# Performance work log

Measured on AMD Instinct MI355X. Metric: run time of the kernel, lower is better.

## Reference

```python
import jax, jax.numpy as jnp
import numpy as np

DILATION = 512
C_RES = 128
C_SKIP = 256


def setup_inputs() -> dict:
    key = jax.random.key(0)
    ks = jax.random.split(key, 6)
    B, T = 8, 16384
    x = jax.random.normal(ks[0], (B, C_RES, T), dtype=jnp.float32)
    # dilated conv weight: [out_ch, in_ch, kernel=2], no bias
    w_dil = jax.random.normal(ks[1], (C_RES, C_RES, 2), dtype=jnp.float32) * (1.0 / np.sqrt(2 * C_RES))
    # 1x1 residual conv (with bias)
    w_res = jax.random.normal(ks[2], (C_RES, C_RES), dtype=jnp.float32) * (1.0 / np.sqrt(C_RES))
    b_res = jax.random.normal(ks[3], (C_RES,), dtype=jnp.float32) * 0.01
    # 1x1 skip conv (with bias)
    w_skip = jax.random.normal(ks[4], (C_SKIP, C_RES), dtype=jnp.float32) * (1.0 / np.sqrt(C_RES))
    b_skip = jax.random.normal(ks[5], (C_SKIP,), dtype=jnp.float32) * 0.01
    return {"x": x, "w_dil": w_dil, "w_res": w_res, "b_res": b_res,
            "w_skip": w_skip, "b_skip": b_skip, "skip_size": 4096}


def reference(x, w_dil, w_res, b_res, w_skip, b_skip, skip_size):
    # x: [B, C, T]. Dilated causal conv, kernel_size=2, dilation=DILATION, no padding:
    # pre[:, :, t] = W[:,:,0] @ x[:,:,t] + W[:,:,1] @ x[:,:,t+DILATION], t in [0, T-DILATION)
    T = x.shape[2]
    L = T - DILATION  # output length
    pre = (jnp.einsum('oi,bit->bot', w_dil[:, :, 0], x[:, :, :L]) +
           jnp.einsum('oi,bit->bot', w_dil[:, :, 1], x[:, :, DILATION:]))
    activated = jnp.tanh(pre) * jax.nn.sigmoid(pre)  # filter * gate
    # 1x1 residual conv + residual add with the time-aligned tail of x
    out = (jnp.einsum('oi,bit->bot', w_res, activated) + b_res[None, :, None]
           + x[:, :, T - L:])
    # 1x1 skip conv, keep last skip_size steps
    skip = jnp.einsum('oi,bit->bot', w_skip, activated) + b_skip[None, :, None]
    skip = skip[:, :, -skip_size:]
    return (out, skip)
```

## Files before the change

### kernel.cpp

```cpp
#include <hip/hip_runtime.h>

typedef float f32x4 __attribute__((ext_vector_type(4)));
typedef __bf16 bf16x8 __attribute__((ext_vector_type(8)));

__device__ __forceinline__ unsigned short f2bf(float f) {
  unsigned u = __builtin_bit_cast(unsigned, f);
  u = (u + 0x7FFFu + ((u >> 16) & 1u)) >> 16;
  return (unsigned short)u;
}

__device__ __forceinline__ f32x4 MFMA16(uint4 a, uint4 b, f32x4 c) {
  return __builtin_amdgcn_mfma_f32_16x16x32_bf16(
      __builtin_bit_cast(bf16x8, a), __builtin_bit_cast(bf16x8, b), c, 0, 0, 0);
}

__global__ void wn_prep(const float* __restrict__ wd, const float* __restrict__ wres,
                        const float* __restrict__ wskip, unsigned short* __restrict__ ws16) {
  int g = blockIdx.x * 256 + threadIdx.x;
  if (g < 40960) {
    int kc = g / 5120, rem = g - kc * 5120;
    int o = rem / 40, c = rem - o * 40;
    float v = 0.f;
    if (c < 32) {
      int k = kc * 32 + c;
      int tap = k >> 7, i = k & 127;
      v = wd[(o << 8) + (i << 1) + tap];
    }
    ws16[g] = f2bf(v);
  } else {
    int g2 = g - 40960;
    int p = g2 / 17408, rem = g2 - p * 17408;
    int r = rem / 136, c = rem - r * 136;
    float v = 0.f;
    if (c < 128) {
      if (p == 0) v = wres[(r << 7) + c];
      else        v = wskip[(((p - 1) << 7) + r) * 128 + c];
    }
    ws16[40960 + g2] = f2bf(v);
  }
}

__global__ __launch_bounds__(512, 4) void wn_main(
    const float* __restrict__ x,
    const float* __restrict__ bres_g,
    const float* __restrict__ bskip_g,
    const unsigned short* __restrict__ wd_img,
    const unsigned short* __restrict__ wrs_img,
    float* __restrict__ out,
    float* __restrict__ skipo) {
  extern __shared__ unsigned short lds[];
  unsigned short* xls  = lds;
  unsigned short* wls  = lds + 10240;
  unsigned short* actT = lds + 20480;
  unsigned short* wrsb = lds;

  const int tile = blockIdx.x;
  const int b = blockIdx.y;
  const int t0 = tile * 128;
  const int tid = threadIdx.x;
  const int lane = tid & 63;
  const int wv = tid >> 6;
  const int mw = wv >> 2;
  const int nw = wv & 3;
  const int l15 = lane & 15;
  const int lhi = lane >> 4;

  const int kq = tid & 7;
  const int tpr = tid >> 3;

  const float* xb_base = x + (size_t)b * (128 * 16384);

  float2 xr[4];
  uint4 wreg0, wreg1;

  auto loadX = [&](int kc) {
    int kglob = kc * 32 + kq * 4;
    int tap = kglob >> 7;
    int ib = kglob & 127;
    const float* p = xb_base + (size_t)ib * 16384 + (t0 + tap * 512 + tpr * 2);
    xr[0] = *(const float2*)(p);
    xr[1] = *(const float2*)(p + 16384);
    xr[2] = *(const float2*)(p + 32768);
    xr[3] = *(const float2*)(p + 49152);
  };
  auto writeX = [&](int buf) {
    unsigned short* dst = xls + buf * 5120;
    int r0 = tpr * 2;
    ushort4 a0, a1;
    a0.x = f2bf(xr[0].x); a0.y = f2bf(xr[1].x); a0.z = f2bf(xr[2].x); a0.w = f2bf(xr[3].x);
    a1.x = f2bf(xr[0].y); a1.y = f2bf(xr[1].y); a1.z = f2bf(xr[2].y); a1.w = f2bf(xr[3].y);
    *(ushort4*)(dst + r0 * 40 + kq * 4) = a0;
    *(ushort4*)(dst + (r0 + 1) * 40 + kq * 4) = a1;
  };
  auto loadW = [&](int kc) {
    const uint4* src = (const uint4*)(wd_img + kc * 5120);
    wreg0 = src[tid];
    if (tid < 128) wreg1 = src[tid + 512];
  };
  auto writeW = [&](int buf) {
    uint4* dst = (uint4*)(wls + buf * 5120);
    dst[tid] = wreg0;
    if (tid < 128) dst[tid + 512] = wreg1;
  };

  f32x4 acc[4][2];
#pragma unroll
  for (int i = 0; i < 4; ++i)
#pragma unroll
    for (int j = 0; j < 2; ++j) acc[i][j] = (f32x4){0.f, 0.f, 0.f, 0.f};

  loadX(0); loadW(0);
  writeX(0); writeW(0);
  __syncthreads();

  for (int kc = 0; kc < 8; ++kc) {
    const int buf = kc & 1;
    if (kc < 7) { loadX(kc + 1); loadW(kc + 1); }
    const unsigned short* wb = wls + buf * 5120;
    const unsigned short* xb = xls + buf * 5120;
    uint4 af[4], bfr[2];
#pragma unroll
    for (int mi = 0; mi < 4; ++mi)
      af[mi] = *(const uint4*)(wb + (mw * 64 + mi * 16 + l15) * 40 + lhi * 8);
#pragma unroll
    for (int ni = 0; ni < 2; ++ni)
      bfr[ni] = *(const uint4*)(xb + (nw * 32 + ni * 16 + l15) * 40 + lhi * 8);
#pragma unroll
    for (int mi = 0; mi < 4; ++mi)
#pragma unroll
      for (int ni = 0; ni < 2; ++ni)
        acc[mi][ni] = MFMA16(af[mi], bfr[ni], acc[mi][ni]);
    if (kc < 7) { writeX(buf ^ 1); writeW(buf ^ 1); }
    __syncthreads();
  }

#pragma unroll
  for (int mi = 0; mi < 4; ++mi) {
#pragma unroll
    for (int ni = 0; ni < 2; ++ni) {
      ushort4 av;
#pragma unroll
      for (int r = 0; r < 4; ++r) {
        float p = acc[mi][ni][r];
        p = fminf(fmaxf(p, -15.f), 15.f);
        float ep = __expf(p);
        float e2 = ep * ep;
        float sg = ep * __builtin_amdgcn_rcpf(1.f + ep);
        float th = (e2 - 1.f) * __builtin_amdgcn_rcpf(e2 + 1.f);
        ((unsigned short*)&av)[r] = f2bf(th * sg);
      }
      int trow = nw * 32 + ni * 16 + l15;
      int o0 = mw * 64 + mi * 16 + lhi * 4;
      *(ushort4*)(actT + trow * 136 + o0) = av;
    }
  }

  const int npass = (tile >= 92) ? 3 : 1;
  for (int p = 0; p < npass; ++p) {
    {
      const uint4* src = (const uint4*)(wrs_img + p * 17408);
      uint4* dst = (uint4*)wrsb;
      for (int u = tid; u < 2176; u += 512) dst[u] = src[u];
    }
    __syncthreads();

    f32x4 acc2[4][2];
#pragma unroll
    for (int i = 0; i < 4; ++i)
#pragma unroll
      for (int j = 0; j < 2; ++j) acc2[i][j] = (f32x4){0.f, 0.f, 0.f, 0.f};

#pragma unroll
    for (int kk = 0; kk < 4; ++kk) {
      uint4 af[4], bfr[2];
#pragma unroll
      for (int mi = 0; mi < 4; ++mi)
        af[mi] = *(const uint4*)(wrsb + (mw * 64 + mi * 16 + l15) * 136 + kk * 32 + lhi * 8);
#pragma unroll
      for (int ni = 0; ni < 2; ++ni)
        bfr[ni] = *(const uint4*)(actT + (nw * 32 + ni * 16 + l15) * 136 + kk * 32 + lhi * 8);
#pragma unroll
      for (int mi = 0; mi < 4; ++mi)
#pragma unroll
        for (int ni = 0; ni < 2; ++ni)
          acc2[mi][ni] = MFMA16(af[mi], bfr[ni], acc2[mi][ni]);
    }

    if (p == 0) {
#pragma unroll
      for (int mi = 0; mi < 4; ++mi) {
        int o0 = mw * 64 + mi * 16 + lhi * 4;
        float br[4];
#pragma unroll
        for (int r = 0; r < 4; ++r) br[r] = bres_g[o0 + r];
#pragma unroll
        for (int ni = 0; ni < 2; ++ni) {
          int tl = nw * 32 + ni * 16 + l15;
#pragma unroll
          for (int r = 0; r < 4; ++r) {
            size_t row = (size_t)(b * 128 + o0 + r);
            float v = acc2[mi][ni][r] + br[r] + x[row * 16384 + 512 + t0 + tl];
            out[row * 15872 + t0 + tl] = v;
          }
        }
      }
    } else {
#pragma unroll
      for (int mi = 0; mi < 4; ++mi) {
        int o2 = (p - 1) * 128 + mw * 64 + mi * 16 + lhi * 4;
        float bs[4];
#pragma unroll
        for (int r = 0; r < 4; ++r) bs[r] = bskip_g[o2 + r];
#pragma unroll
        for (int ni = 0; ni < 2; ++ni) {
          int tl = nw * 32 + ni * 16 + l15;
          int s = t0 + tl - 11776;
#pragma unroll
          for (int r = 0; r < 4; ++r) {
            skipo[(size_t)(b * 256 + o2 + r) * 4096 + s] = acc2[mi][ni][r] + bs[r];
          }
        }
      }
    }
    __syncthreads();
  }
}

extern "C" void kernel_launch(void* const* d_in, const int* in_sizes, int n_in,
                              void* d_out, int out_size, void* d_ws, size_t ws_size,
                              hipStream_t stream) {
  const float* x      = (const float*)d_in[0];
  const float* w_dil  = (const float*)d_in[1];
  const float* w_res  = (const float*)d_in[2];
  const float* b_res  = (const float*)d_in[3];
  const float* w_skip = (const float*)d_in[4];
  const float* b_skip = (const float*)d_in[5];
  unsigned short* ws16 = (unsigned short*)d_ws;
  float* out = (float*)d_out;
  float* skipo = out + 16252928;

  wn_prep<<<364, 256, 0, stream>>>(w_dil, w_res, w_skip, ws16);

  dim3 grid(124, 8);
  wn_main<<<grid, 512, 75776, stream>>>(x, b_res, b_skip, ws16, ws16 + 40960, out, skipo);
}
```

Measured before the change: 85.01 us.

## Deepen global load prefetch to three chunks in register ring buffer

```diff
diff --git a/kernel.cpp b/kernel.cpp
--- a/kernel.cpp
+++ b/kernel.cpp
@@ -70,38 +70,36 @@
 
   const float* xb_base = x + (size_t)b * (128 * 16384);
 
-  float2 xr[4];
-  uint4 wreg0, wreg1;
-
-  auto loadX = [&](int kc) {
-    int kglob = kc * 32 + kq * 4;
+  float2 xr[3][4];
+  uint4  wr0[3];
+  unsigned wr1[3];
+
+  auto issueChunk = [&](int c) {
+    int s = c % 3;
+    int kglob = c * 32 + kq * 4;
     int tap = kglob >> 7;
     int ib = kglob & 127;
     const float* p = xb_base + (size_t)ib * 16384 + (t0 + tap * 512 + tpr * 2);
-    xr[0] = *(const float2*)(p);
-    xr[1] = *(const float2*)(p + 16384);
-    xr[2] = *(const float2*)(p + 32768);
-    xr[3] = *(const float2*)(p + 49152);
+    xr[s][0] = *(const float2*)(p);
+    xr[s][1] = *(const float2*)(p + 16384);
+    xr[s][2] = *(const float2*)(p + 32768);
+    xr[s][3] = *(const float2*)(p + 49152);
+    wr0[s] = ((const uint4*)(wd_img + c * 5120))[tid];
+    wr1[s] = ((const unsigned*)(wd_img + c * 5120))[2048 + tid];
   };
-  auto writeX = [&](int buf) {
+  auto writeChunk = [&](int c, int buf) {
+    int s = c % 3;
     unsigned short* dst = xls + buf * 5120;
     int r0 = tpr * 2;
     ushort4 a0, a1;
-    a0.x = f2bf(xr[0].x); a0.y = f2bf(xr[1].x); a0.z = f2bf(xr[2].x); a0.w = f2bf(xr[3].x);
-    a1.x = f2bf(xr[0].y); a1.y = f2bf(xr[1].y); a1.z = f2bf(xr[2].y); a1.w = f2bf(xr[3].y);
+    a0.x = f2bf(xr[s][0].x); a0.y = f2bf(xr[s][1].x); a0.z = f2bf(xr[s][2].x); a0.w = f2bf(xr[s][3].x);
+    a1.x = f2bf(xr[s][0].y); a1.y = f2bf(xr[s][1].y); a1.z = f2bf(xr[s][2].y); a1.w = f2bf(xr[s][3].y);
     *(ushort4*)(dst + r0 * 40 + kq * 4) = a0;
     *(ushort4*)(dst + (r0 + 1) * 40 + kq * 4) = a1;
+    unsigned short* wdst = wls + buf * 5120;
+    ((uint4*)wdst)[tid] = wr0[s];
+    ((unsigned*)wdst)[2048 + tid] = wr1[s];
   };
-  auto loadW = [&](int kc) {
-    const uint4* src = (const uint4*)(wd_img + kc * 5120);
-    wreg0 = src[tid];
-    if (tid < 128) wreg1 = src[tid + 512];
-  };
-  auto writeW = [&](int buf) {
-    uint4* dst = (uint4*)(wls + buf * 5120);
-    dst[tid] = wreg0;
-    if (tid < 128) dst[tid + 512] = wreg1;
-  };
 
   f32x4 acc[4][2];
 #pragma unroll
@@ -109,13 +107,14 @@
 #pragma unroll
     for (int j = 0; j < 2; ++j) acc[i][j] = (f32x4){0.f, 0.f, 0.f, 0.f};
 
-  loadX(0); loadW(0);
-  writeX(0); writeW(0);
+  issueChunk(0); issueChunk(1); issueChunk(2);
+  writeChunk(0, 0);
   __syncthreads();
 
+#pragma unroll
   for (int kc = 0; kc < 8; ++kc) {
     const int buf = kc & 1;
-    if (kc < 7) { loadX(kc + 1); loadW(kc + 1); }
+    if (kc + 3 < 8) issueChunk(kc + 3);
     const unsigned short* wb = wls + buf * 5120;
     const unsigned short* xb = xls + buf * 5120;
     uint4 af[4], bfr[2];
@@ -130,7 +129,7 @@
 #pragma unroll
       for (int ni = 0; ni < 2; ++ni)
         acc[mi][ni] = MFMA16(af[mi], bfr[ni], acc[mi][ni]);
-    if (kc < 7) { writeX(buf ^ 1); writeW(buf ^ 1); }
+    if (kc < 7) writeChunk(kc + 1, buf ^ 1);
     __syncthreads();
   }
 
@@ -160,7 +159,11 @@
     {
       const uint4* src = (const uint4*)(wrs_img + p * 17408);
       uint4* dst = (uint4*)wrsb;
-      for (int u = tid; u < 2176; u += 512) dst[u] = src[u];
+      dst[tid] = src[tid];
+      dst[tid + 512] = src[tid + 512];
+      dst[tid + 1024] = src[tid + 1024];
+      dst[tid + 1536] = src[tid + 1536];
+      if (tid < 128) dst[tid + 2048] = src[tid + 2048];
     }
     __syncthreads();
 
```

Measured after the change: 91.77 us. 8.0% more time.

## Halve time tile and stream residual/skip weights in double-buffered K-chunks

Applied to the files above, without the earlier changes.

```diff
diff --git a/kernel.cpp b/kernel.cpp
--- a/kernel.cpp
+++ b/kernel.cpp
@@ -29,39 +29,39 @@
     ws16[g] = f2bf(v);
   } else {
     int g2 = g - 40960;
-    int p = g2 / 17408, rem = g2 - p * 17408;
-    int r = rem / 136, c = rem - r * 136;
-    float v = 0.f;
-    if (c < 128) {
-      if (p == 0) v = wres[(r << 7) + c];
-      else        v = wskip[(((p - 1) << 7) + r) * 128 + c];
-    }
+    int pkk = g2 >> 12;
+    int rem = g2 & 4095;
+    int o = rem >> 5, kl = rem & 31;
+    int p = pkk >> 2, kk = pkk & 3;
+    int k = kk * 32 + kl;
+    float v = (p == 0) ? wres[o * 128 + k] : wskip[((p - 1) * 128 + o) * 128 + k];
     ws16[40960 + g2] = f2bf(v);
   }
 }
 
-__global__ __launch_bounds__(512, 4) void wn_main(
+__global__ __launch_bounds__(256, 4) void wn_main(
     const float* __restrict__ x,
     const float* __restrict__ bres_g,
     const float* __restrict__ bskip_g,
     const unsigned short* __restrict__ wd_img,
-    const unsigned short* __restrict__ wrs_img,
+    const unsigned short* __restrict__ wrs2_img,
     float* __restrict__ out,
     float* __restrict__ skipo) {
   extern __shared__ unsigned short lds[];
   unsigned short* xls  = lds;
-  unsigned short* wls  = lds + 10240;
-  unsigned short* actT = lds + 20480;
-  unsigned short* wrsb = lds;
-
-  const int tile = blockIdx.x;
-  const int b = blockIdx.y;
-  const int t0 = tile * 128;
+  unsigned short* actT = lds;
+  unsigned short* wls  = lds + 8704;
+
+  const int w = blockIdx.x;
+  const int b = w & 7;
+  const int tile = w >> 3;
+  const int t0 = tile * 64;
+
   const int tid = threadIdx.x;
   const int lane = tid & 63;
   const int wv = tid >> 6;
-  const int mw = wv >> 2;
-  const int nw = wv & 3;
+  const int mw = wv >> 1;
+  const int nw = wv & 1;
   const int l15 = lane & 15;
   const int lhi = lane >> 4;
 
@@ -71,9 +71,9 @@
   const float* xb_base = x + (size_t)b * (128 * 16384);
 
   float2 xr[4];
-  uint4 wreg0, wreg1;
-
-  auto loadX = [&](int kc) {
+  uint4 wrA, wrB, wrC;
+
+  auto issueX = [&](int kc) {
     int kglob = kc * 32 + kq * 4;
     int tap = kglob >> 7;
     int ib = kglob & 127;
@@ -84,7 +84,7 @@
     xr[3] = *(const float2*)(p + 49152);
   };
   auto writeX = [&](int buf) {
-    unsigned short* dst = xls + buf * 5120;
+    unsigned short* dst = xls + buf * 2560;
     int r0 = tpr * 2;
     ushort4 a0, a1;
     a0.x = f2bf(xr[0].x); a0.y = f2bf(xr[1].x); a0.z = f2bf(xr[2].x); a0.w = f2bf(xr[3].x);
@@ -92,15 +92,28 @@
     *(ushort4*)(dst + r0 * 40 + kq * 4) = a0;
     *(ushort4*)(dst + (r0 + 1) * 40 + kq * 4) = a1;
   };
-  auto loadW = [&](int kc) {
+  auto loadW1 = [&](int kc) {
     const uint4* src = (const uint4*)(wd_img + kc * 5120);
-    wreg0 = src[tid];
-    if (tid < 128) wreg1 = src[tid + 512];
-  };
-  auto writeW = [&](int buf) {
+    wrA = src[tid];
+    wrB = src[tid + 256];
+    if (tid < 128) wrC = src[tid + 512];
+  };
+  auto writeW1 = [&](int buf) {
     uint4* dst = (uint4*)(wls + buf * 5120);
-    dst[tid] = wreg0;
-    if (tid < 128) dst[tid + 512] = wreg1;
+    dst[tid] = wrA;
+    dst[tid + 256] = wrB;
+    if (tid < 128) dst[tid + 512] = wrC;
+  };
+  auto loadW2 = [&](int p, int kk) {
+    const uint4* src = (const uint4*)(wrs2_img + ((p * 4 + kk) << 12));
+    wrA = src[tid];
+    wrB = src[tid + 256];
+  };
+  auto writeW2 = [&](int buf) {
+    unsigned short* base = wls + buf * 5120;
+    int u0 = tid, u1 = tid + 256;
+    *(uint4*)(base + (u0 >> 2) * 40 + (u0 & 3) * 8) = wrA;
+    *(uint4*)(base + (u1 >> 2) * 40 + (u1 & 3) * 8) = wrB;
   };
 
   f32x4 acc[4][2];
@@ -109,28 +122,29 @@
 #pragma unroll
     for (int j = 0; j < 2; ++j) acc[i][j] = (f32x4){0.f, 0.f, 0.f, 0.f};
 
-  loadX(0); loadW(0);
-  writeX(0); writeW(0);
+  issueX(0); loadW1(0);
+  writeX(0); writeW1(0);
   __syncthreads();
 
+#pragma unroll
   for (int kc = 0; kc < 8; ++kc) {
     const int buf = kc & 1;
-    if (kc < 7) { loadX(kc + 1); loadW(kc + 1); }
-    const unsigned short* wb = wls + buf * 5120;
-    const unsigned short* xb = xls + buf * 5120;
+    if (kc < 7) { issueX(kc + 1); loadW1(kc + 1); }
+    const unsigned short* wbuf = wls + buf * 5120;
+    const unsigned short* xbuf = xls + buf * 2560;
     uint4 af[4], bfr[2];
 #pragma unroll
     for (int mi = 0; mi < 4; ++mi)
-      af[mi] = *(const uint4*)(wb + (mw * 64 + mi * 16 + l15) * 40 + lhi * 8);
+      af[mi] = *(const uint4*)(wbuf + (mw * 64 + mi * 16 + l15) * 40 + lhi * 8);
 #pragma unroll
     for (int ni = 0; ni < 2; ++ni)
-      bfr[ni] = *(const uint4*)(xb + (nw * 32 + ni * 16 + l15) * 40 + lhi * 8);
+      bfr[ni] = *(const uint4*)(xbuf + (nw * 32 + ni * 16 + l15) * 40 + lhi * 8);
 #pragma unroll
     for (int mi = 0; mi < 4; ++mi)
 #pragma unroll
       for (int ni = 0; ni < 2; ++ni)
         acc[mi][ni] = MFMA16(af[mi], bfr[ni], acc[mi][ni]);
-    if (kc < 7) { writeX(buf ^ 1); writeW(buf ^ 1); }
+    if (kc < 7) { writeX(buf ^ 1); writeW1(buf ^ 1); }
     __syncthreads();
   }
 
@@ -155,13 +169,10 @@
     }
   }
 
-  const int npass = (tile >= 92) ? 3 : 1;
+  const int npass = (tile >= 184) ? 3 : 1;
   for (int p = 0; p < npass; ++p) {
-    {
-      const uint4* src = (const uint4*)(wrs_img + p * 17408);
-      uint4* dst = (uint4*)wrsb;
-      for (int u = tid; u < 2176; u += 512) dst[u] = src[u];
-    }
+    loadW2(p, 0);
+    writeW2(0);
     __syncthreads();
 
     f32x4 acc2[4][2];
@@ -172,10 +183,13 @@
 
 #pragma unroll
     for (int kk = 0; kk < 4; ++kk) {
+      const int buf = kk & 1;
+      if (kk < 3) loadW2(p, kk + 1);
+      const unsigned short* wbuf = wls + buf * 5120;
       uint4 af[4], bfr[2];
 #pragma unroll
       for (int mi = 0; mi < 4; ++mi)
-        af[mi] = *(const uint4*)(wrsb + (mw * 64 + mi * 16 + l15) * 136 + kk * 32 + lhi * 8);
+        af[mi] = *(const uint4*)(wbuf + (mw * 64 + mi * 16 + l15) * 40 + lhi * 8);
 #pragma unroll
       for (int ni = 0; ni < 2; ++ni)
         bfr[ni] = *(const uint4*)(actT + (nw * 32 + ni * 16 + l15) * 136 + kk * 32 + lhi * 8);
@@ -184,6 +198,8 @@
 #pragma unroll
         for (int ni = 0; ni < 2; ++ni)
           acc2[mi][ni] = MFMA16(af[mi], bfr[ni], acc2[mi][ni]);
+      if (kk < 3) writeW2(buf ^ 1);
+      __syncthreads();
     }
 
     if (p == 0) {
@@ -222,7 +238,6 @@
         }
       }
     }
-    __syncthreads();
   }
 }
 
@@ -239,8 +254,7 @@
   float* out = (float*)d_out;
   float* skipo = out + 16252928;
 
-  wn_prep<<<364, 256, 0, stream>>>(w_dil, w_res, w_skip, ws16);
-
-  dim3 grid(124, 8);
-  wn_main<<<grid, 512, 75776, stream>>>(x, b_res, b_skip, ws16, ws16 + 40960, out, skipo);
-}
+  wn_prep<<<352, 256, 0, stream>>>(w_dil, w_res, w_skip, ws16);
+
+  wn_main<<<1984, 256, 37888, stream>>>(x, b_res, b_skip, ws16, ws16 + 40960, out, skipo);
+}
```

Result: faster. 81.94 us (-3.6%).
